# Performance work log

Hardware: AMD Instinct MI355X
Metric: run time of the kernel (lower is better)

## Reference

```python
import jax, jax.numpy as jnp
import numpy as np

MARGIN = 0.2
SIMILARITY_WEIGHT = 1.0
PD_EPS = 1e-6   # F.pairwise_distance eps (added to the difference)
COS_EPS = 1e-8  # F.cosine_similarity eps (norm clamp)

B, D = 8192, 256


def setup_inputs() -> dict:
    key = jax.random.key(0)
    k1, k2, k3, k4 = jax.random.split(key, 4)
    anchor = jax.random.normal(k1, (B, D), dtype=jnp.float32)
    positive = jax.random.normal(k2, (B, D), dtype=jnp.float32)
    negative = jax.random.normal(k3, (B, D), dtype=jnp.float32)
    similarity_matrix = jax.random.uniform(k4, (B, B), dtype=jnp.float32)
    return {"anchor": anchor, "positive": positive, "negative": negative,
            "similarity_matrix": similarity_matrix}


def reference(anchor, positive, negative, similarity_matrix):
    # Triplet term: F.pairwise_distance(x1, x2, p=2, eps=1e-6) = ||x1 - x2 + eps||_2
    d_pos = jnp.linalg.norm(anchor - positive + PD_EPS, axis=1)  # [B]
    d_neg = jnp.linalg.norm(anchor - negative + PD_EPS, axis=1)  # [B]
    triplet = jnp.mean(jax.nn.relu(d_pos - d_neg + MARGIN))

    # Pairwise cosine similarity of anchor rows (vectorized matmul form).
    norms = jnp.linalg.norm(anchor, axis=1, keepdims=True)       # [B,1]
    a_hat = anchor / jnp.maximum(norms, COS_EPS)                 # [B,D]
    cos = a_hat @ a_hat.T                                        # [B,B]

    # sum_{i,j} mse(cos_ij, S_ij) / B^2 == mean((cos - S)^2)
    sim_loss = jnp.mean((cos - similarity_matrix) ** 2)

    return triplet + SIMILARITY_WEIGHT * sim_loss
```

## Files before the change

kernel.cpp:

```cpp
#include <hip/hip_runtime.h>
#include <hip/hip_bf16.h>

#define BDIM 8192
#define DDIM 256

typedef __attribute__((ext_vector_type(8))) short  s16x8;
typedef __attribute__((ext_vector_type(4))) float  f32x4;

#define GLOBAL_AS __attribute__((address_space(1)))
#define LDS_AS    __attribute__((address_space(3)))

__device__ __forceinline__ void stage16nt(const float* g, float* l) {
    __builtin_amdgcn_global_load_lds((const GLOBAL_AS unsigned int*)g,
                                     (LDS_AS unsigned int*)l, 16, 0, 2 );
}

__device__ inline ushort f2bf(float x) {
    __hip_bfloat16 h = __float2bfloat16(x);
    ushort u;
    __builtin_memcpy(&u, &h, 2);
    return u;
}

__global__ __launch_bounds__(256) void row_stats(
    const float* __restrict__ A, const float* __restrict__ P,
    const float* __restrict__ N, ushort* __restrict__ Asw,
    float* __restrict__ partial_trip)
{
    __shared__ float tsh[4];
    const int wave = threadIdx.x >> 6;
    const int lane = threadIdx.x & 63;
    const int row  = blockIdx.x * 4 + wave;

    const float4 a = *(reinterpret_cast<const float4*>(A + (size_t)row * DDIM) + lane);
    const float4 p = *(reinterpret_cast<const float4*>(P + (size_t)row * DDIM) + lane);
    const float4 n = *(reinterpret_cast<const float4*>(N + (size_t)row * DDIM) + lane);

    float sa = a.x*a.x + a.y*a.y + a.z*a.z + a.w*a.w;

    float d0 = a.x - p.x + 1e-6f, d1 = a.y - p.y + 1e-6f;
    float d2 = a.z - p.z + 1e-6f, d3 = a.w - p.w + 1e-6f;
    float sp = d0*d0 + d1*d1 + d2*d2 + d3*d3;

    d0 = a.x - n.x + 1e-6f; d1 = a.y - n.y + 1e-6f;
    d2 = a.z - n.z + 1e-6f; d3 = a.w - n.w + 1e-6f;
    float sn = d0*d0 + d1*d1 + d2*d2 + d3*d3;

    #pragma unroll
    for (int off = 32; off > 0; off >>= 1) {
        sa += __shfl_xor(sa, off);
        sp += __shfl_xor(sp, off);
        sn += __shfl_xor(sn, off);
    }

    const float inv = 1.0f / fmaxf(sqrtf(sa), 1e-8f);

    ushort4 hv;
    hv.x = f2bf(a.x * inv);
    hv.y = f2bf(a.y * inv);
    hv.z = f2bf(a.z * inv);
    hv.w = f2bf(a.w * inv);
    const size_t chunk = ((size_t)(row >> 4) * 8 + (lane >> 3)) * 64
                       + (size_t)(((lane >> 1) & 3) * 16 + (row & 15));
    *reinterpret_cast<ushort4*>(Asw + chunk * 8 + (lane & 1) * 4) = hv;

    if (lane == 0)
        tsh[wave] = fmaxf(sqrtf(sp) - sqrtf(sn) + 0.2f, 0.0f);
    __syncthreads();
    if (threadIdx.x == 0)
        partial_trip[blockIdx.x] = tsh[0] + tsh[1] + tsh[2] + tsh[3];
}

__global__ __launch_bounds__(256, 2) void cos_mse(
    const ushort* __restrict__ Asw,
    const float* __restrict__ S,
    float* __restrict__ partial_sim)
{
    __shared__ float s_tile[128 * 128];

    const int tid  = threadIdx.x;
    const int w    = tid >> 6;
    const int lane = tid & 63;

    const int b   = blockIdx.x;
    const int xcd = b & 7;
    const int q   = b >> 3;
    const int ti  = (xcd * 8 + (q >> 3)) * 128;

    const int wr    = (w >> 1) * 64;
    const int wc    = (w & 1) * 64;
    const int fr    = lane & 15;
    const int kg    = lane >> 4;
    const int rhalf = lane >> 5;
    const int col16 = lane & 31;

    s16x8 af[32];
    {
        const ushort* ab = Asw + (size_t)((ti + wr) >> 4) * 4096 + (size_t)lane * 8;
        #pragma unroll
        for (int k32 = 0; k32 < 8; ++k32)
            #pragma unroll
            for (int m = 0; m < 4; ++m)
                af[k32 * 4 + m] = *reinterpret_cast<const s16x8*>(
                    ab + (size_t)m * 4096 + k32 * 512);
    }

    for (int i = 0; i < 8; ++i) {
        const int tj = ((q & 7) * 8 + i) * 128;

        {
            const float* gsrc = S + (size_t)(ti + w * 2 + rhalf) * BDIM + tj + col16 * 4;
            #pragma unroll
            for (int it = 0; it < 16; ++it)
                stage16nt(gsrc + (size_t)it * 8 * BDIM,
                          &s_tile[(it * 8 + w * 2) * 128]);
        }

        f32x4 acc[4][4] = {};
        const ushort* bb = Asw + (size_t)((tj + wc) >> 4) * 4096 + (size_t)lane * 8;
        #pragma unroll
        for (int k32 = 0; k32 < 8; ++k32) {
            s16x8 bf4[4];
            #pragma unroll
            for (int n = 0; n < 4; ++n)
                bf4[n] = *reinterpret_cast<const s16x8*>(
                    bb + (size_t)n * 4096 + k32 * 512);
            #pragma unroll
            for (int m = 0; m < 4; ++m)
                #pragma unroll
                for (int n = 0; n < 4; ++n)
                    acc[m][n] = __builtin_amdgcn_mfma_f32_16x16x32_bf16(
                        af[k32 * 4 + m], bf4[n], acc[m][n], 0, 0, 0);
        }

        __syncthreads();

        float local = 0.0f;
        #pragma unroll
        for (int m = 0; m < 4; ++m)
            #pragma unroll
            for (int reg = 0; reg < 4; ++reg) {
                const int lr = wr + m * 16 + kg * 4 + reg;
                #pragma unroll
                for (int n = 0; n < 4; ++n) {
                    const float d = acc[m][n][reg]
                                  - s_tile[lr * 128 + wc + n * 16 + fr];
                    local += d * d;
                }
            }

        #pragma unroll
        for (int off = 32; off > 0; off >>= 1)
            local += __shfl_down(local, off);
        if (lane == 0)
            partial_sim[(size_t)(xcd * 512 + q * 8 + i) * 4 + w] = local;

        __syncthreads();
    }
}

__global__ __launch_bounds__(256) void finalize(
    const float* __restrict__ pt, const float* __restrict__ ps,
    float* __restrict__ out)
{
    __shared__ float sh[4];
    float v = 0.0f;
    for (int i = threadIdx.x; i < 2048; i += 256)
        v += pt[i] * (1.0f / (float)BDIM);
    for (int i = threadIdx.x; i < 16384; i += 256)
        v += ps[i] * (1.0f / ((float)BDIM * (float)BDIM));
    #pragma unroll
    for (int off = 32; off > 0; off >>= 1) v += __shfl_down(v, off);
    const int w = threadIdx.x >> 6, lane = threadIdx.x & 63;
    if (lane == 0) sh[w] = v;
    __syncthreads();
    if (threadIdx.x == 0) out[0] = sh[0] + sh[1] + sh[2] + sh[3];
}

extern "C" void kernel_launch(void* const* d_in, const int* in_sizes, int n_in,
                              void* d_out, int out_size, void* d_ws, size_t ws_size,
                              hipStream_t stream)
{
    const float* anchor   = (const float*)d_in[0];
    const float* positive = (const float*)d_in[1];
    const float* negative = (const float*)d_in[2];
    const float* S        = (const float*)d_in[3];
    float* out = (float*)d_out;

    float*  partial_trip = (float*)d_ws;
    float*  partial_sim  = (float*)((char*)d_ws + 8192);
    ushort* Asw          = (ushort*)((char*)d_ws + 131072);

    row_stats<<<BDIM / 4, 256, 0, stream>>>(anchor, positive, negative, Asw, partial_trip);
    cos_mse<<<512, 256, 0, stream>>>(Asw, S, partial_sim);
    finalize<<<1, 256, 0, stream>>>(partial_trip, partial_sim, out);
}
```

Baseline: 100.4 us.

## Load similarity tile directly to registers and drop LDS staging

The similarity-matrix tile is no longer staged through a 64KB LDS buffer with async global-to-LDS loads. Each lane now reads the S values matching its MFMA accumulator layout straight into registers with nontemporal loads. A-fragments are reloaded from global or cache on every k-step instead of being held in 32 registers, and partial sums are kept per block rather than per tile, which shrinks the workspace and the finalize loop. The aim is to drop LDS usage and the barriers and raise occupancy, at the cost of strided, less-coalesced S reads (16 floats per row segment) and repeated A loads.

```diff
diff --git a/kernel.cpp b/kernel.cpp
--- a/kernel.cpp
+++ b/kernel.cpp
@@ -6,14 +6,6 @@
 
 typedef __attribute__((ext_vector_type(8))) short  s16x8;
 typedef __attribute__((ext_vector_type(4))) float  f32x4;
-
-#define GLOBAL_AS __attribute__((address_space(1)))
-#define LDS_AS    __attribute__((address_space(3)))
-
-__device__ __forceinline__ void stage16nt(const float* g, float* l) {
-    __builtin_amdgcn_global_load_lds((const GLOBAL_AS unsigned int*)g,
-                                     (LDS_AS unsigned int*)l, 16, 0, 2 );
-}
 
 __device__ inline ushort f2bf(float x) {
     __hip_bfloat16 h = __float2bfloat16(x);
@@ -76,8 +68,6 @@
     const float* __restrict__ S,
     float* __restrict__ partial_sim)
 {
-    __shared__ float s_tile[128 * 128];
-
     const int tid  = threadIdx.x;
     const int w    = tid >> 6;
     const int lane = tid & 63;
@@ -87,76 +77,70 @@
     const int q   = b >> 3;
     const int ti  = (xcd * 8 + (q >> 3)) * 128;
 
-    const int wr    = (w >> 1) * 64;
-    const int wc    = (w & 1) * 64;
-    const int fr    = lane & 15;
-    const int kg    = lane >> 4;
-    const int rhalf = lane >> 5;
-    const int col16 = lane & 31;
+    const int wr = (w >> 1) * 64;
+    const int wc = (w & 1) * 64;
+    const int fr = lane & 15;
+    const int kg = lane >> 4;
 
-    s16x8 af[32];
-    {
-        const ushort* ab = Asw + (size_t)((ti + wr) >> 4) * 4096 + (size_t)lane * 8;
-        #pragma unroll
-        for (int k32 = 0; k32 < 8; ++k32)
-            #pragma unroll
-            for (int m = 0; m < 4; ++m)
-                af[k32 * 4 + m] = *reinterpret_cast<const s16x8*>(
-                    ab + (size_t)m * 4096 + k32 * 512);
-    }
+    const ushort* ab = Asw + (size_t)((ti + wr) >> 4) * 4096 + (size_t)lane * 8;
+
+    float local = 0.0f;
 
     for (int i = 0; i < 8; ++i) {
         const int tj = ((q & 7) * 8 + i) * 128;
-
-        {
-            const float* gsrc = S + (size_t)(ti + w * 2 + rhalf) * BDIM + tj + col16 * 4;
-            #pragma unroll
-            for (int it = 0; it < 16; ++it)
-                stage16nt(gsrc + (size_t)it * 8 * BDIM,
-                          &s_tile[(it * 8 + w * 2) * 128]);
-        }
+        const ushort* bb = Asw + (size_t)((tj + wc) >> 4) * 4096 + (size_t)lane * 8;
 
         f32x4 acc[4][4] = {};
-        const ushort* bb = Asw + (size_t)((tj + wc) >> 4) * 4096 + (size_t)lane * 8;
-        #pragma unroll
+        #pragma unroll 2
         for (int k32 = 0; k32 < 8; ++k32) {
-            s16x8 bf4[4];
+            s16x8 afr[4], bfr[4];
+            #pragma unroll
+            for (int m = 0; m < 4; ++m)
+                afr[m] = *reinterpret_cast<const s16x8*>(
+                    ab + (size_t)m * 4096 + k32 * 512);
             #pragma unroll
             for (int n = 0; n < 4; ++n)
-                bf4[n] = *reinterpret_cast<const s16x8*>(
+                bfr[n] = *reinterpret_cast<const s16x8*>(
                     bb + (size_t)n * 4096 + k32 * 512);
             #pragma unroll
             for (int m = 0; m < 4; ++m)
                 #pragma unroll
                 for (int n = 0; n < 4; ++n)
                     acc[m][n] = __builtin_amdgcn_mfma_f32_16x16x32_bf16(
-                        af[k32 * 4 + m], bf4[n], acc[m][n], 0, 0, 0);
+                        afr[m], bfr[n], acc[m][n], 0, 0, 0);
         }
 
-        __syncthreads();
+        __builtin_amdgcn_sched_barrier(0);
 
-        float local = 0.0f;
+        const float* sbase = S + (size_t)(ti + wr + kg * 4) * BDIM + tj + wc + fr;
+        float sv[4][4][4];
         #pragma unroll
         for (int m = 0; m < 4; ++m)
             #pragma unroll
-            for (int reg = 0; reg < 4; ++reg) {
-                const int lr = wr + m * 16 + kg * 4 + reg;
+            for (int reg = 0; reg < 4; ++reg)
+                #pragma unroll
+                for (int n = 0; n < 4; ++n)
+                    sv[m][reg][n] = __builtin_nontemporal_load(
+                        sbase + (size_t)(m * 16 + reg) * BDIM + n * 16);
+
+        __builtin_amdgcn_sched_barrier(0);
+
+        #pragma unroll
+        for (int m = 0; m < 4; ++m)
+            #pragma unroll
+            for (int reg = 0; reg < 4; ++reg)
                 #pragma unroll
                 for (int n = 0; n < 4; ++n) {
-                    const float d = acc[m][n][reg]
-                                  - s_tile[lr * 128 + wc + n * 16 + fr];
+                    const float d = acc[m][n][reg] - sv[m][reg][n];
                     local += d * d;
                 }
-            }
+    }
 
-        #pragma unroll
-        for (int off = 32; off > 0; off >>= 1)
-            local += __shfl_down(local, off);
-        if (lane == 0)
-            partial_sim[(size_t)(xcd * 512 + q * 8 + i) * 4 + w] = local;
-
-        __syncthreads();
-    }
+    #pragma unroll
+    for (int off = 32; off > 0; off >>= 1)
+        local += __shfl_down(local, off);
+    if (lane == 0)
+        partial_sim[b * 4 + w] = local;
 }
 
 __global__ __launch_bounds__(256) void finalize(
@@ -167,7 +151,7 @@
     float v = 0.0f;
     for (int i = threadIdx.x; i < 2048; i += 256)
         v += pt[i] * (1.0f / (float)BDIM);
-    for (int i = threadIdx.x; i < 16384; i += 256)
+    for (int i = threadIdx.x; i < 2048; i += 256)
         v += ps[i] * (1.0f / ((float)BDIM * (float)BDIM));
     #pragma unroll
     for (int off = 32; off > 0; off >>= 1) v += __shfl_down(v, off);
@@ -189,7 +173,7 @@
 
     float*  partial_trip = (float*)d_ws;
     float*  partial_sim  = (float*)((char*)d_ws + 8192);
-    ushort* Asw          = (ushort*)((char*)d_ws + 131072);
+    ushort* Asw          = (ushort*)((char*)d_ws + 32768);
 
     row_stats<<<BDIM / 4, 256, 0, stream>>>(anchor, positive, negative, Asw, partial_trip);
     cos_mse<<<512, 256, 0, stream>>>(Asw, S, partial_sim);
```

New measurement: 108.5 us. +8.0%, slower.
